# Kernel optimization log

Hardware: AMD Instinct MI355X
Metric: run time of the kernel (lower is better)

Reference implementation:

```python
import jax, jax.numpy as jnp
import numpy as np

N_GAS_NETS = 76  # 29 h2o + 13 o3 + 9 co2 + 3 n2o + 9 ch4 + 13 uniform
N_CHANNELS = 29
N_IN = 2   # (temperature, pressure)
H = 64     # hidden width per n_hidden=[64,64]

# gas index (into composition[0..5]) for each of the 76 stacked nets
COMP_IDX = jnp.asarray(np.repeat(np.arange(6), [29, 13, 9, 3, 9, 13]))

# sparse per-channel combine (hard-coded in the original forward)
H2O_IDX = jnp.asarray([0,1,2,3,4,5,6,3,4,9,10,11,12,13,14,15,16,17,18,19,20,21,22,23,24,25,26,27,28])
O3_CH  = jnp.asarray([0,1,2,17,18,19,20,21,22,25,26,27,28])
CO2_CH = jnp.asarray([0,1,2,5,6,9,10,13,14])
N2O_CH = jnp.asarray([0,1,2])
CH4_CH = jnp.asarray([0,1,2,3,4,7,8,11,12])
U_CH   = jnp.asarray([0,1,2,15,16,17,18,19,20,21,22,27,28])


def setup_inputs() -> dict:
    key = jax.random.key(0)
    ks = jax.random.split(key, 10)
    N = 32768
    t_p = jax.random.normal(ks[0], (N, N_IN), dtype=jnp.float32)
    composition = jax.random.uniform(ks[1], (8, N, 1), dtype=jnp.float32)
    s1 = 1.0 / np.sqrt(N_IN)
    s2 = 1.0 / np.sqrt(H)
    W1 = jax.random.normal(ks[2], (N_GAS_NETS, N_IN, H), dtype=jnp.float32) * s1
    b1 = jnp.zeros((N_GAS_NETS, H), dtype=jnp.float32)
    W2 = jax.random.normal(ks[3], (N_GAS_NETS, H, H), dtype=jnp.float32) * s2
    b2 = jnp.zeros((N_GAS_NETS, H), dtype=jnp.float32)
    Wout = jax.random.normal(ks[4], (N_GAS_NETS, H, 1), dtype=jnp.float32) * s2
    bout = jnp.zeros((N_GAS_NETS, 1), dtype=jnp.float32)
    ke_lw = jax.random.uniform(ks[5], (N_CHANNELS, 1), dtype=jnp.float32)
    ke_iw = jax.random.uniform(ks[6], (N_CHANNELS, 1), dtype=jnp.float32)
    return {"t_p": t_p, "composition": composition, "W1": W1, "b1": b1,
            "W2": W2, "b2": b2, "Wout": Wout, "bout": bout,
            "ke_lw": ke_lw, "ke_iw": ke_iw}


def reference(t_p, composition, W1, b1, W2, b2, Wout, bout, ke_lw, ke_iw):
    # Batched evaluation of all 76 tiny DenseFFN experts on the shared t_p input.
    h = jax.nn.relu(jnp.einsum('ni,gih->gnh', t_p, W1) + b1[:, None, :])   # [76,N,H]
    h = jax.nn.relu(jnp.einsum('gnh,ghk->gnk', h, W2) + b2[:, None, :])    # [76,N,H]
    ke = jax.nn.relu(jnp.einsum('gnh,gho->gno', h, Wout) + bout[:, None, :])  # [76,N,1]

    # tau_gas[gas] = ke * composition[gas_index]
    tau_all = ke * composition[COMP_IDX]  # [76,N,1]
    h2o = tau_all[0:29]
    o3 = tau_all[29:42]
    co2 = tau_all[42:51]
    n2o = tau_all[51:54]
    ch4 = tau_all[54:63]
    u = tau_all[63:76]

    # hard-coded sparse per-channel sum
    tau_gases = h2o[H2O_IDX]                      # [29,N,1]
    tau_gases = tau_gases.at[O3_CH].add(o3)
    tau_gases = tau_gases.at[CO2_CH].add(co2)
    tau_gases = tau_gases.at[N2O_CH].add(n2o)
    tau_gases = tau_gases.at[CH4_CH].add(ch4)
    tau_gases = tau_gases.at[U_CH].add(u)

    tau_lw = ke_lw[:, None, :] * composition[6]   # [29,N,1]
    tau_iw = ke_iw[:, None, :] * composition[7]   # [29,N,1]
    return (tau_gases, tau_lw, tau_iw)
```

## Files before the change

kernel.cpp:

```cpp
#include <hip/hip_runtime.h>

#define NPTS 32768

typedef _Float16 f16;
typedef _Float16 f16x2 __attribute__((ext_vector_type(2)));
typedef _Float16 f16x8 __attribute__((ext_vector_type(8)));
typedef float f32x2 __attribute__((ext_vector_type(2)));
typedef float f32x4 __attribute__((ext_vector_type(4)));

union H8 { f16x8 v8; f16x2 v2[4]; };

static __device__ __forceinline__ f16x2 pk_fma(f16x2 a, f16x2 b, f16x2 c) {
  return __builtin_elementwise_fma(a, b, c);
}
static __device__ __forceinline__ f16x2 pk_relu(f16x2 a) {
  f16x2 z = {(f16)0.f, (f16)0.f};
  return __builtin_elementwise_max(a, z);
}

__device__ const unsigned char G_T[74] = {
  0,0,0,0,0,0,0, 0,0,0,0,0,0,0,0,0,0,0,0,0,0,0,0,0,0,0,0,
  1,1,1,1,1,1,1,1,1,1,1,1,1,
  2,2,2,2,2,2,2,2,2,
  3,3,3,
  4,4,4,4,4,4,4,4,4,
  5,5,5,5,5,5,5,5,5,5,5,5,5
};
__device__ const unsigned char G_C1[74] = {
  0,1,2,3,4,5,6, 9,10,11,12,13,14,15,16,17,18,19,20,21,22,23,24,25,26,27,28,
  0,1,2,17,18,19,20,21,22,25,26,27,28,
  0,1,2,5,6,9,10,13,14,
  0,1,2,
  0,1,2,3,4,7,8,11,12,
  0,1,2,15,16,17,18,19,20,21,22,27,28
};
__device__ const unsigned char G_C2[74] = {
  255,255,255,7,8,255,255, 255,255,255,255,255,255,255,255,255,255,255,255,
  255,255,255,255,255,255,255,255,
  255,255,255,255,255,255,255,255,255,255,255,255,255,
  255,255,255,255,255,255,255,255,255,
  255,255,255,
  255,255,255,255,255,255,255,255,255,
  255,255,255,255,255,255,255,255,255,255,255,255,255
};

__global__ __launch_bounds__(256) void k0_init(
    const float* __restrict__ comp, const float* __restrict__ ke_lw,
    const float* __restrict__ ke_iw, float* __restrict__ out)
{
  const int c = blockIdx.x >> 7;
  const int n = ((blockIdx.x & 127) << 8) + threadIdx.x;
  out[c * NPTS + n] = 0.f;
  out[29 * NPTS + c * NPTS + n] = ke_lw[c] * comp[6 * NPTS + n];
  out[58 * NPTS + c * NPTS + n] = ke_iw[c] * comp[7 * NPTS + n];
}

__global__ __launch_bounds__(256, 2) void k1_mlp(
    const float* __restrict__ t_p, const float* __restrict__ comp,
    const float* __restrict__ W1, const float* __restrict__ b1,
    const float* __restrict__ W2, const float* __restrict__ b2,
    const float* __restrict__ Wout, const float* __restrict__ bout,
    float* __restrict__ out)
{
  const int lane = threadIdx.x & 63;
  const int l15  = lane & 15;
  const int quad = lane >> 4;
  const int w    = blockIdx.x * 4 + (threadIdx.x >> 6);
  const int gi   = w >> 6;
  const int g    = gi + (gi >= 7 ? 2 : 0);
  const int pb0  = (w & 63) * 512;

  const int t  = G_T[gi];
  const int c1 = G_C1[gi];
  const int c2 = G_C2[gi];

  H8 afrag[4][2];
  const float* W2g = W2 + g * 4096;
  #pragma unroll
  for (int mt = 0; mt < 4; ++mt) {
    #pragma unroll
    for (int ks = 0; ks < 2; ++ks) {
      const float* src = W2g + (ks * 32 + quad * 8) * 64 + mt * 16 + l15;
      #pragma unroll
      for (int i = 0; i < 4; ++i) {
        f16x2 tt = { (f16)src[(2 * i) * 64], (f16)src[(2 * i + 1) * 64] };
        afrag[mt][ks].v2[i] = tt;
      }
    }
  }

  f16x2 w0h[2][4], w1h[2][4], b1h[2][4];
  const float* W1g = W1 + g * 128;
  const float* b1g = b1 + g * 64;
  #pragma unroll
  for (int ks = 0; ks < 2; ++ks) {
    #pragma unroll
    for (int i = 0; i < 4; ++i) {
      int h = ks * 32 + quad * 8 + 2 * i;
      w0h[ks][i] = f16x2{ (f16)W1g[h],      (f16)W1g[h + 1] };
      w1h[ks][i] = f16x2{ (f16)W1g[64 + h], (f16)W1g[64 + h + 1] };
      b1h[ks][i] = f16x2{ (f16)b1g[h],      (f16)b1g[h + 1] };
    }
  }

  f32x4 b2q[4];
  f32x2 wq2[4][2];
  #pragma unroll
  for (int mt = 0; mt < 4; ++mt) {
    b2q[mt] = *(const f32x4*)(b2 + g * 64 + mt * 16 + quad * 4);
    f32x4 wv = *(const f32x4*)(Wout + g * 64 + mt * 16 + quad * 4);
    wq2[mt][0] = f32x2{ wv[0], wv[1] };
    wq2[mt][1] = f32x2{ wv[2], wv[3] };
  }
  const float bo = bout[g];

  const float2* tp2 = (const float2*)t_p;
  const float* compt = comp + t * NPTS;
  float* out1 = out + c1 * NPTS;
  float* out2 = (c2 == 255) ? nullptr : out + c2 * NPTS;

  for (int pass = 0; pass < 8; ++pass) {
    const int pb = pb0 + pass * 64;

    float2 xv[4];
    #pragma unroll
    for (int pt = 0; pt < 4; ++pt)
      xv[pt] = tp2[pb + pt * 16 + l15];
    const float cv = compt[pb + lane];

    f16x2 x0v[4], x1v[4];
    #pragma unroll
    for (int pt = 0; pt < 4; ++pt) {
      f16 x0 = (f16)xv[pt].x, x1 = (f16)xv[pt].y;
      x0v[pt] = f16x2{ x0, x0 };
      x1v[pt] = f16x2{ x1, x1 };
    }

    H8 bfrag[2][4];
    #pragma unroll
    for (int ks = 0; ks < 2; ++ks)
      #pragma unroll
      for (int pt = 0; pt < 4; ++pt)
        #pragma unroll
        for (int i = 0; i < 4; ++i)
          bfrag[ks][pt].v2[i] =
              pk_relu(pk_fma(x0v[pt], w0h[ks][i], pk_fma(x1v[pt], w1h[ks][i], b1h[ks][i])));

    f32x4 acc[4][4];
    #pragma unroll
    for (int mt = 0; mt < 4; ++mt)
      #pragma unroll
      for (int pt = 0; pt < 4; ++pt) {
        f32x4 c0 = __builtin_amdgcn_mfma_f32_16x16x32_f16(
            afrag[mt][0].v8, bfrag[0][pt].v8, b2q[mt], 0, 0, 0);
        acc[mt][pt] = __builtin_amdgcn_mfma_f32_16x16x32_f16(
            afrag[mt][1].v8, bfrag[1][pt].v8, c0, 0, 0, 0);
      }

    float ke[4];
    #pragma unroll
    for (int pt = 0; pt < 4; ++pt) {
      f32x2 p2 = { 0.f, 0.f };
      #pragma unroll
      for (int mt = 0; mt < 4; ++mt) {
        f32x2 z = { 0.f, 0.f };
        f32x2 a0 = { acc[mt][pt][0], acc[mt][pt][1] };
        f32x2 a1 = { acc[mt][pt][2], acc[mt][pt][3] };
        a0 = __builtin_elementwise_max(a0, z);
        a1 = __builtin_elementwise_max(a1, z);
        p2 = __builtin_elementwise_fma(a0, wq2[mt][0], p2);
        p2 = __builtin_elementwise_fma(a1, wq2[mt][1], p2);
      }
      float p = p2[0] + p2[1];
      p += __shfl_xor(p, 16, 64);
      p += __shfl_xor(p, 32, 64);
      ke[pt] = fmaxf(p + bo, 0.f);
    }
    float v = (quad == 0) ? ke[0] : (quad == 1) ? ke[1] : (quad == 2) ? ke[2] : ke[3];
    float tau = v * cv;
    atomicAdd(&out1[pb + lane], tau);
    if (out2) atomicAdd(&out2[pb + lane], tau);
  }
}

extern "C" void kernel_launch(void* const* d_in, const int* in_sizes, int n_in,
                              void* d_out, int out_size, void* d_ws, size_t ws_size,
                              hipStream_t stream)
{
  const float* t_p   = (const float*)d_in[0];
  const float* comp  = (const float*)d_in[1];
  const float* W1    = (const float*)d_in[2];
  const float* b1    = (const float*)d_in[3];
  const float* W2    = (const float*)d_in[4];
  const float* b2    = (const float*)d_in[5];
  const float* Wout  = (const float*)d_in[6];
  const float* bout  = (const float*)d_in[7];
  const float* ke_lw = (const float*)d_in[8];
  const float* ke_iw = (const float*)d_in[9];
  float* out = (float*)d_out;

  k0_init<<<29 * 128, 256, 0, stream>>>(comp, ke_lw, ke_iw, out);
  k1_mlp<<<1184, 256, 0, stream>>>(t_p, comp, W1, b1, W2, b2, Wout, bout, out);
}
```

Measured before the change: 113.8 us.

## Split MLP work across more waves and use transpose-reduce for output sums

Each wave now processes 128 points in two unrolled passes instead of 512 in eight, and the grid is four times larger. This spreads the work over more waves to help latency hiding and load balance. The per-point cross-quad reduction now uses a butterfly transpose, so three shuffles replace eight per pass. Packed round-toward-zero f32-to-f16 conversion replaces scalar casts. The trade-off is that W2 and W1 fragments are reloaded and converted four times as often, because each wave does less work per weight load.

```diff
diff --git a/kernel.cpp b/kernel.cpp
--- a/kernel.cpp
+++ b/kernel.cpp
@@ -16,6 +16,9 @@
 static __device__ __forceinline__ f16x2 pk_relu(f16x2 a) {
   f16x2 z = {(f16)0.f, (f16)0.f};
   return __builtin_elementwise_max(a, z);
+}
+static __device__ __forceinline__ f16x2 pk_cvt(float a, float b) {
+  return __builtin_bit_cast(f16x2, __builtin_amdgcn_cvt_pkrtz(a, b));
 }
 
 __device__ const unsigned char G_T[74] = {
@@ -66,14 +69,17 @@
   const int l15  = lane & 15;
   const int quad = lane >> 4;
   const int w    = blockIdx.x * 4 + (threadIdx.x >> 6);
-  const int gi   = w >> 6;
+  const int gi   = w >> 8;
   const int g    = gi + (gi >= 7 ? 2 : 0);
-  const int pb0  = (w & 63) * 512;
+  const int pb0  = (w & 255) * 128;
 
   const int t  = G_T[gi];
   const int c1 = G_C1[gi];
   const int c2 = G_C2[gi];
 
+  const bool qb0 = (quad & 1) != 0;
+  const bool qb1 = (quad & 2) != 0;
+
   H8 afrag[4][2];
   const float* W2g = W2 + g * 4096;
   #pragma unroll
@@ -82,10 +88,8 @@
     for (int ks = 0; ks < 2; ++ks) {
       const float* src = W2g + (ks * 32 + quad * 8) * 64 + mt * 16 + l15;
       #pragma unroll
-      for (int i = 0; i < 4; ++i) {
-        f16x2 tt = { (f16)src[(2 * i) * 64], (f16)src[(2 * i + 1) * 64] };
-        afrag[mt][ks].v2[i] = tt;
-      }
+      for (int i = 0; i < 4; ++i)
+        afrag[mt][ks].v2[i] = pk_cvt(src[(2 * i) * 64], src[(2 * i + 1) * 64]);
     }
   }
 
@@ -97,9 +101,9 @@
     #pragma unroll
     for (int i = 0; i < 4; ++i) {
       int h = ks * 32 + quad * 8 + 2 * i;
-      w0h[ks][i] = f16x2{ (f16)W1g[h],      (f16)W1g[h + 1] };
-      w1h[ks][i] = f16x2{ (f16)W1g[64 + h], (f16)W1g[64 + h + 1] };
-      b1h[ks][i] = f16x2{ (f16)b1g[h],      (f16)b1g[h + 1] };
+      w0h[ks][i] = pk_cvt(W1g[h],      W1g[h + 1]);
+      w1h[ks][i] = pk_cvt(W1g[64 + h], W1g[64 + h + 1]);
+      b1h[ks][i] = pk_cvt(b1g[h],      b1g[h + 1]);
     }
   }
 
@@ -119,7 +123,8 @@
   float* out1 = out + c1 * NPTS;
   float* out2 = (c2 == 255) ? nullptr : out + c2 * NPTS;
 
-  for (int pass = 0; pass < 8; ++pass) {
+  #pragma unroll
+  for (int pass = 0; pass < 2; ++pass) {
     const int pb = pb0 + pass * 64;
 
     float2 xv[4];
@@ -131,9 +136,8 @@
     f16x2 x0v[4], x1v[4];
     #pragma unroll
     for (int pt = 0; pt < 4; ++pt) {
-      f16 x0 = (f16)xv[pt].x, x1 = (f16)xv[pt].y;
-      x0v[pt] = f16x2{ x0, x0 };
-      x1v[pt] = f16x2{ x1, x1 };
+      x0v[pt] = pk_cvt(xv[pt].x, xv[pt].x);
+      x1v[pt] = pk_cvt(xv[pt].y, xv[pt].y);
     }
 
     H8 bfrag[2][4];
@@ -157,7 +161,7 @@
             afrag[mt][1].v8, bfrag[1][pt].v8, c0, 0, 0, 0);
       }
 
-    float ke[4];
+    float p[4];
     #pragma unroll
     for (int pt = 0; pt < 4; ++pt) {
       f32x2 p2 = { 0.f, 0.f };
@@ -171,13 +175,18 @@
         p2 = __builtin_elementwise_fma(a0, wq2[mt][0], p2);
         p2 = __builtin_elementwise_fma(a1, wq2[mt][1], p2);
       }
-      float p = p2[0] + p2[1];
-      p += __shfl_xor(p, 16, 64);
-      p += __shfl_xor(p, 32, 64);
-      ke[pt] = fmaxf(p + bo, 0.f);
-    }
-    float v = (quad == 0) ? ke[0] : (quad == 1) ? ke[1] : (quad == 2) ? ke[2] : ke[3];
-    float tau = v * cv;
+      p[pt] = p2[0] + p2[1];
+    }
+
+    float u = qb1 ? (qb0 ? p[3] : p[2]) : (qb0 ? p[1] : p[0]);
+    float v = qb1 ? (qb0 ? p[2] : p[3]) : (qb0 ? p[0] : p[1]);
+    float wv2 = qb1 ? (qb0 ? p[1] : p[0]) : (qb0 ? p[3] : p[2]);
+    float x = qb1 ? (qb0 ? p[0] : p[1]) : (qb0 ? p[2] : p[3]);
+    float s = u + __shfl_xor(v, 16, 64);
+    float tt = wv2 + __shfl_xor(x, 16, 64);
+    float r = s + __shfl_xor(tt, 32, 64);
+
+    float tau = fmaxf(r + bo, 0.f) * cv;
     atomicAdd(&out1[pb + lane], tau);
     if (out2) atomicAdd(&out2[pb + lane], tau);
   }
@@ -200,5 +209,5 @@
   float* out = (float*)d_out;
 
   k0_init<<<29 * 128, 256, 0, stream>>>(comp, ke_lw, ke_iw, out);
-  k1_mlp<<<1184, 256, 0, stream>>>(t_p, comp, W1, b1, W2, b2, Wout, bout, out);
-}
+  k1_mlp<<<4736, 256, 0, stream>>>(t_p, comp, W1, b1, W2, b2, Wout, bout, out);
+}
```

Result: slower. 121.2 us (+6.5%).
